# Kernel tuning notes

Hardware: AMD Instinct MI355X
Metric: run time of the kernel (lower is better)

Reference implementation:

```python
import jax, jax.numpy as jnp
import numpy as np

ALPHA = 0.01  # alpha = input_scale * weight_scale (dequant scale)
BETA = 1.0    # bias scale, fixed to 1.0 in forward


def setup_inputs() -> dict:
    key = jax.random.key(0)
    k1, k2, k3 = jax.random.split(key, 3)
    # int8 values carried in int32 containers (schema has no int8 dtype)
    x = jax.random.randint(k1, (2, 2048, 4096), -127, 128, dtype=jnp.int32)
    weight = jax.random.randint(k2, (11008, 4096), -127, 128, dtype=jnp.int32)
    bias = jax.random.normal(k3, (1, 11008), dtype=jnp.float32)
    return {"x": x, "weight": weight, "bias": bias}


def reference(x, weight, bias):
    # x: [..., K] int8 activations, weight: [N, K] int8, bias: [1, N] fp32
    x_shape = x.shape
    x2 = x.reshape(-1, x_shape[-1]).astype(jnp.int8)   # [M, K]
    w8 = weight.astype(jnp.int8)                        # [N, K]
    acc = jnp.einsum('mk,nk->mn', x2, w8, preferred_element_type=jnp.int32)
    # fused dequant scale + fp32 bias add
    y = ALPHA * acc.astype(jnp.float32) + BETA * bias   # [M, N]
    return y.reshape(*x_shape[:-1], -1)
```

## Files before the change

kernel.cpp:

```cpp
#include <hip/hip_runtime.h>


#define M_DIM 4096
#define N_DIM 11008
#define K_DIM 4096
#define BM 256
#define BN 128
#define BK 64
#define ALPHA 0.01f

typedef __attribute__((ext_vector_type(4))) int i32x4;

static __device__ __forceinline__ int pack4(int4 v) {
    return (v.x & 0xff) | ((v.y & 0xff) << 8) |
           ((v.z & 0xff) << 16) | ((unsigned)(v.w & 0xff) << 24);
}

__global__ __launch_bounds__(256) void pack_i8_kernel(
    const int4* __restrict__ x, int4* __restrict__ xout, int n16x,
    const int4* __restrict__ w, int4* __restrict__ wout, int n16_total)
{
    int i = blockIdx.x * blockDim.x + threadIdx.x;
    if (i >= n16_total) return;
    const int4* src;
    int4* dst;
    int idx;
    if (i < n16x) { src = x; dst = xout; idx = i; }
    else          { src = w; dst = wout; idx = i - n16x; }
    const int4* p = src + (size_t)4 * idx;
    int4 a = p[0], b = p[1], c = p[2], d = p[3];
    int4 r;
    r.x = pack4(a); r.y = pack4(b); r.z = pack4(c); r.w = pack4(d);
    dst[idx] = r;
}

__global__ __launch_bounds__(256, 2) void gemm_i8_kernel(
    const char* __restrict__ A,
    const char* __restrict__ B,
    const float* __restrict__ bias,
    float* __restrict__ C)
{
    __shared__ __attribute__((aligned(16))) char As[BM * BK];
    __shared__ __attribute__((aligned(16))) char Bs[BN * BK];

    const int tid  = threadIdx.x;
    const int lane = tid & 63;
    const int wave = tid >> 6;
    const int waveM = (wave >> 1) * 128;
    const int waveN = (wave & 1) * 64;
    const int bm = blockIdx.y * BM;
    const int bn = blockIdx.x * BN;

    const int lrow  = lane & 15;
    const int lquad = lane >> 4;

    const int srow = tid >> 2;
    const int scol = ((tid & 3) ^ ((tid >> 3) & 3)) * 16;
    const char* Abase = A + (size_t)(bm + srow) * K_DIM + scol;
    const char* Bbase = B + (size_t)(bn + srow) * K_DIM + scol;

    const int swq = (lquad ^ ((lrow >> 1) & 3)) * 16;

    i32x4 acc[8][4] = {};

    for (int k0 = 0; k0 < K_DIM; k0 += BK) {
#pragma unroll
        for (int c = 0; c < 4; c++)
            __builtin_amdgcn_global_load_lds(
                (const __attribute__((address_space(1))) void*)(Abase + (size_t)(64 * c) * K_DIM + k0),
                (__attribute__((address_space(3))) void*)(As + c * 4096 + tid * 16), 16, 0, 0);
#pragma unroll
        for (int c = 0; c < 2; c++)
            __builtin_amdgcn_global_load_lds(
                (const __attribute__((address_space(1))) void*)(Bbase + (size_t)(64 * c) * K_DIM + k0),
                (__attribute__((address_space(3))) void*)(Bs + c * 4096 + tid * 16), 16, 0, 0);
        __syncthreads();

        i32x4 a[8], b[4];
#pragma unroll
        for (int i = 0; i < 8; i++)
            a[i] = *(const i32x4*)(As + (waveM + i * 16 + lrow) * BK + swq);
#pragma unroll
        for (int j = 0; j < 4; j++)
            b[j] = *(const i32x4*)(Bs + (waveN + j * 16 + lrow) * BK + swq);

#pragma unroll
        for (int i = 0; i < 8; i++)
#pragma unroll
            for (int j = 0; j < 4; j++)
                acc[i][j] = __builtin_amdgcn_mfma_i32_16x16x64_i8(a[i], b[j], acc[i][j], 0, 0, 0);

        __syncthreads();
    }

#pragma unroll
    for (int i = 0; i < 8; i++) {
        const int r0 = bm + waveM + i * 16 + lquad * 4;
#pragma unroll
        for (int j = 0; j < 4; j++) {
            const int c0 = bn + waveN + j * 16 + lrow;
            const float bv = bias[c0];
#pragma unroll
            for (int r = 0; r < 4; r++) {
                C[(size_t)(r0 + r) * N_DIM + c0] = ALPHA * (float)acc[i][j][r] + bv;
            }
        }
    }
}

extern "C" void kernel_launch(void* const* d_in, const int* in_sizes, int n_in,
                              void* d_out, int out_size, void* d_ws, size_t ws_size,
                              hipStream_t stream) {
    const int*   x    = (const int*)d_in[0];
    const int*   w    = (const int*)d_in[1];
    const float* bias = (const float*)d_in[2];
    float*       out  = (float*)d_out;

    char* Ap = (char*)d_ws;
    char* Wp = (char*)d_ws + (size_t)M_DIM * K_DIM;

    const int n16x = M_DIM * K_DIM / 16;
    const int n16w = N_DIM * K_DIM / 16;
    const int n16  = n16x + n16w;
    pack_i8_kernel<<<n16 / 256, 256, 0, stream>>>(
        (const int4*)x, (int4*)Ap, n16x, (const int4*)w, (int4*)Wp, n16);

    dim3 grid(N_DIM / BN, M_DIM / BM);
    gemm_i8_kernel<<<grid, 256, 0, stream>>>(Ap, Wp, bias, out);
}
```

Measured before the change: 550.5 us.

## Double-buffer 256x256x128 int8 GEMM tiles with staged loads and XCD-aware block mapping

Grows the GEMM block tile to 256x256 with BK=128 and moves to 512 threads (8 waves). LDS becomes double-buffered, and the global-to-LDS loads for the next K tile are interleaved with four MFMA quadrant phases, using barriers, explicit vmcnt waits and s_setprio. Blocks are remapped to a 1D grid so that each XCD handles neighbouring M rows, for better L2 reuse. The aim is to hide load latency and raise arithmetic intensity, at the cost of 128KB of LDS per block and more registers, which limits occupancy.

```diff
diff --git a/kernel.cpp b/kernel.cpp
--- a/kernel.cpp
+++ b/kernel.cpp
@@ -5,8 +5,9 @@
 #define N_DIM 11008
 #define K_DIM 4096
 #define BM 256
-#define BN 128
-#define BK 64
+#define BN 256
+#define BK 128
+#define NT (K_DIM / BK)
 #define ALPHA 0.01f
 
 typedef __attribute__((ext_vector_type(4))) int i32x4;
@@ -34,63 +35,135 @@
     dst[idx] = r;
 }
 
-__global__ __launch_bounds__(256, 2) void gemm_i8_kernel(
+#define GLOAD_LDS16(g, l) __builtin_amdgcn_global_load_lds(                   \
+    (const __attribute__((address_space(1))) void*)(g),                       \
+    (__attribute__((address_space(3))) void*)(l), 16, 0, 0)
+
+#define MFMA_Q(mh, nh, aq, bq)                                                \
+    __builtin_amdgcn_s_setprio(1);                                            \
+    _Pragma("unroll")                                                         \
+    for (int i_ = 0; i_ < 4; i_++)                                            \
+        _Pragma("unroll")                                                     \
+        for (int j_ = 0; j_ < 2; j_++)                                        \
+            _Pragma("unroll")                                                 \
+            for (int k_ = 0; k_ < 2; k_++)                                    \
+                acc[(mh) * 4 + i_][(nh) * 2 + j_] =                           \
+                    __builtin_amdgcn_mfma_i32_16x16x64_i8(                    \
+                        aq[i_][k_], bq[j_][k_],                               \
+                        acc[(mh) * 4 + i_][(nh) * 2 + j_], 0, 0, 0);          \
+    __builtin_amdgcn_s_setprio(0);
+
+__global__ __launch_bounds__(512, 2) void gemm_i8_kernel(
     const char* __restrict__ A,
     const char* __restrict__ B,
     const float* __restrict__ bias,
     float* __restrict__ C)
 {
-    __shared__ __attribute__((aligned(16))) char As[BM * BK];
-    __shared__ __attribute__((aligned(16))) char Bs[BN * BK];
-
-    const int tid  = threadIdx.x;
-    const int lane = tid & 63;
-    const int wave = tid >> 6;
-    const int waveM = (wave >> 1) * 128;
-    const int waveN = (wave & 1) * 64;
-    const int bm = blockIdx.y * BM;
-    const int bn = blockIdx.x * BN;
-
+    __shared__ __attribute__((aligned(16))) char As[2][BM * BK];
+    __shared__ __attribute__((aligned(16))) char Bs[2][BN * BK];
+
+    const int tid   = threadIdx.x;
+    const int lane  = tid & 63;
+    const int wave  = tid >> 6;
+    const int waveM = (wave >> 2) * 128;
+    const int waveN = (wave & 3) * 64;
     const int lrow  = lane & 15;
     const int lquad = lane >> 4;
 
-    const int srow = tid >> 2;
-    const int scol = ((tid & 3) ^ ((tid >> 3) & 3)) * 16;
-    const char* Abase = A + (size_t)(bm + srow) * K_DIM + scol;
-    const char* Bbase = B + (size_t)(bn + srow) * K_DIM + scol;
-
-    const int swq = (lquad ^ ((lrow >> 1) & 3)) * 16;
+    const int bid = blockIdx.x;
+    const int xcd = bid & 7;
+    const int loc = bid >> 3;
+    const int bm  = (2 * xcd + (loc & 1)) * BM;
+    const int bn  = (loc >> 1) * BN;
+
+    const int srow = tid >> 3;
+    const int schk = ((tid & 7) ^ (srow & 7)) << 4;
+    const char* Asrc = A + (size_t)(bm + srow) * K_DIM + schk;
+    const char* Bsrc = B + (size_t)(bn + srow) * K_DIM + schk;
+
+    int aoff[2], boff[2];
+#pragma unroll
+    for (int ks = 0; ks < 2; ks++) {
+        const int pos = ((ks * 4 + lquad) ^ (lrow & 7)) << 4;
+        aoff[ks] = (waveM + lrow) * BK + pos;
+        boff[ks] = (waveN + lrow) * BK + pos;
+    }
 
     i32x4 acc[8][4] = {};
 
-    for (int k0 = 0; k0 < K_DIM; k0 += BK) {
-#pragma unroll
-        for (int c = 0; c < 4; c++)
-            __builtin_amdgcn_global_load_lds(
-                (const __attribute__((address_space(1))) void*)(Abase + (size_t)(64 * c) * K_DIM + k0),
-                (__attribute__((address_space(3))) void*)(As + c * 4096 + tid * 16), 16, 0, 0);
-#pragma unroll
-        for (int c = 0; c < 2; c++)
-            __builtin_amdgcn_global_load_lds(
-                (const __attribute__((address_space(1))) void*)(Bbase + (size_t)(64 * c) * K_DIM + k0),
-                (__attribute__((address_space(3))) void*)(Bs + c * 4096 + tid * 16), 16, 0, 0);
-        __syncthreads();
-
-        i32x4 a[8], b[4];
-#pragma unroll
-        for (int i = 0; i < 8; i++)
-            a[i] = *(const i32x4*)(As + (waveM + i * 16 + lrow) * BK + swq);
-#pragma unroll
-        for (int j = 0; j < 4; j++)
-            b[j] = *(const i32x4*)(Bs + (waveN + j * 16 + lrow) * BK + swq);
-
-#pragma unroll
-        for (int i = 0; i < 8; i++)
-#pragma unroll
-            for (int j = 0; j < 4; j++)
-                acc[i][j] = __builtin_amdgcn_mfma_i32_16x16x64_i8(a[i], b[j], acc[i][j], 0, 0, 0);
-
-        __syncthreads();
+    auto stage_a = [&](int buf, int t, int half) {
+        GLOAD_LDS16(Asrc + (size_t)(half * 128) * K_DIM + t * BK,
+                    &As[buf][half * 16384 + tid * 16]);
+        GLOAD_LDS16(Asrc + (size_t)(half * 128 + 64) * K_DIM + t * BK,
+                    &As[buf][half * 16384 + 8192 + tid * 16]);
+    };
+    auto stage_b = [&](int buf, int t, int half) {
+        GLOAD_LDS16(Bsrc + (size_t)(half * 128) * K_DIM + t * BK,
+                    &Bs[buf][half * 16384 + tid * 16]);
+        GLOAD_LDS16(Bsrc + (size_t)(half * 128 + 64) * K_DIM + t * BK,
+                    &Bs[buf][half * 16384 + 8192 + tid * 16]);
+    };
+
+    stage_a(0, 0, 0); stage_a(0, 0, 1);
+    stage_b(0, 0, 0); stage_b(0, 0, 1);
+    stage_a(1, 1, 0); stage_a(1, 1, 1);
+    asm volatile("s_waitcnt vmcnt(4)" ::: "memory");
+    __builtin_amdgcn_s_barrier();
+
+    for (int g = 0; g < NT; ++g) {
+        const int cur = g & 1;
+        const char* Ac = As[cur];
+        const char* Bc = Bs[cur];
+        i32x4 a0[4][2], a1[4][2], b01[2][2], b23[2][2];
+
+#pragma unroll
+        for (int i = 0; i < 4; i++)
+#pragma unroll
+            for (int ks = 0; ks < 2; ks++)
+                a0[i][ks] = *(const i32x4*)(Ac + aoff[ks] + i * 2048);
+#pragma unroll
+        for (int j = 0; j < 2; j++)
+#pragma unroll
+            for (int ks = 0; ks < 2; ks++)
+                b01[j][ks] = *(const i32x4*)(Bc + boff[ks] + j * 2048);
+        if (g + 1 < NT) { stage_b(cur ^ 1, g + 1, 0); }
+        __builtin_amdgcn_s_barrier();
+        MFMA_Q(0, 0, a0, b01);
+        __builtin_amdgcn_s_barrier();
+
+#pragma unroll
+        for (int j = 0; j < 2; j++)
+#pragma unroll
+            for (int ks = 0; ks < 2; ks++)
+                b23[j][ks] = *(const i32x4*)(Bc + boff[ks] + (j + 2) * 2048);
+        if (g + 1 < NT) { stage_b(cur ^ 1, g + 1, 1); }
+        __builtin_amdgcn_s_barrier();
+        MFMA_Q(0, 1, a0, b23);
+        __builtin_amdgcn_s_barrier();
+
+#pragma unroll
+        for (int i = 0; i < 4; i++)
+#pragma unroll
+            for (int ks = 0; ks < 2; ks++)
+                a1[i][ks] = *(const i32x4*)(Ac + aoff[ks] + (i + 4) * 2048);
+        __builtin_amdgcn_s_barrier();
+        MFMA_Q(1, 1, a1, b23);
+        __builtin_amdgcn_s_barrier();
+
+#pragma unroll
+        for (int j = 0; j < 2; j++)
+#pragma unroll
+            for (int ks = 0; ks < 2; ks++)
+                b01[j][ks] = *(const i32x4*)(Bc + boff[ks] + j * 2048);
+        if (g + 2 < NT) {
+            stage_a(cur, g + 2, 0); stage_a(cur, g + 2, 1);
+            asm volatile("s_waitcnt vmcnt(4)" ::: "memory");
+        } else {
+            asm volatile("s_waitcnt vmcnt(0)" ::: "memory");
+        }
+        __builtin_amdgcn_s_barrier();
+        MFMA_Q(1, 0, a1, b01);
+        __builtin_amdgcn_s_barrier();
     }
 
 #pragma unroll
@@ -125,6 +198,6 @@
     pack_i8_kernel<<<n16 / 256, 256, 0, stream>>>(
         (const int4*)x, (int4*)Ap, n16x, (const int4*)w, (int4*)Wp, n16);
 
-    dim3 grid(N_DIM / BN, M_DIM / BM);
-    gemm_i8_kernel<<<grid, 256, 0, stream>>>(Ap, Wp, bias, out);
-}
+    gemm_i8_kernel<<<dim3((M_DIM / BM) * (N_DIM / BN)), 512, 0, stream>>>(
+        Ap, Wp, bias, out);
+}
```

Result: no change. 548.5 us (-0.4%).

## Double-buffer LDS with 256x256x128 tiles, interleaved prefetch and XCD-aware block mapping

Applied to the files above, without the earlier changes.

The int8 GEMM is restructured around a 256x256 output tile with a K step of 128, run by 512 threads (8 waves) per block. LDS is double-buffered, and the global-to-LDS loads for the next K tile are split into four chunks. Each chunk is interleaved with MFMA groups, using explicit vmcnt waits, barriers and setprio, so memory traffic overlaps compute instead of the previous load-sync-compute loop. A 1D grid is remapped so that consecutive blocks on each XCD share A rows, and the LDS swizzle is widened to 8 chunks. The trade-off is about 128KB of LDS per block, which limits occupancy to one block per CU, plus a tightly hand-scheduled pipeline whose correctness depends on the wait counts.

```diff
diff --git a/kernel.cpp b/kernel.cpp
--- a/kernel.cpp
+++ b/kernel.cpp
@@ -5,8 +5,9 @@
 #define N_DIM 11008
 #define K_DIM 4096
 #define BM 256
-#define BN 128
-#define BK 64
+#define BN 256
+#define BK 128
+#define NT (K_DIM / BK)
 #define ALPHA 0.01f
 
 typedef __attribute__((ext_vector_type(4))) int i32x4;
@@ -34,64 +35,135 @@
     dst[idx] = r;
 }
 
-__global__ __launch_bounds__(256, 2) void gemm_i8_kernel(
+#define GA0 (s_ + 8 * (s_ >> 3))
+#define GA1 (8 + s_ + 8 * (s_ >> 3))
+#define GB0 ((s_ & 3) + 8 * (s_ >> 2))
+#define GB1 (4 + (s_ & 3) + 8 * (s_ >> 2))
+
+#define STAGE(dstArr, srcB, T, GEXPR)                                          \
+    _Pragma("unroll") for (int u_ = 0; u_ < 2; u_++) {                         \
+        const int s_ = u_ * 8 + wave;                                          \
+        const int G_ = (GEXPR);                                                \
+        __builtin_amdgcn_global_load_lds(                                      \
+            (const __attribute__((address_space(1))) void*)(                   \
+                (srcB) + (size_t)(G_ * 8 + (lane >> 3)) * K_DIM +              \
+                (size_t)(T) * BK + sch16),                                     \
+            (__attribute__((address_space(3))) void*)((dstArr) + G_ * 1024 +   \
+                                                      lane * 16),              \
+            16, 0, 0);                                                         \
+    }
+
+#define READ_A(Arr, dst, IB)                                                   \
+    _Pragma("unroll") for (int i_ = 0; i_ < 4; i_++)                           \
+        _Pragma("unroll") for (int k_ = 0; k_ < 2; k_++)                       \
+            dst[i_][k_] = *(const i32x4*)((Arr) + aoff[k_] + ((IB) + i_) * 2048);
+
+#define READ_B(Arr, dst, JB)                                                   \
+    _Pragma("unroll") for (int j_ = 0; j_ < 2; j_++)                           \
+        _Pragma("unroll") for (int k_ = 0; k_ < 2; k_++)                       \
+            dst[j_][k_] = *(const i32x4*)((Arr) + boff[k_] + ((JB) + j_) * 2048);
+
+#define MFMA_G(af, bf, IB, JB)                                                 \
+    __builtin_amdgcn_s_setprio(1);                                             \
+    _Pragma("unroll") for (int i_ = 0; i_ < 4; i_++)                           \
+        _Pragma("unroll") for (int j_ = 0; j_ < 2; j_++)                       \
+            _Pragma("unroll") for (int k_ = 0; k_ < 2; k_++)                   \
+                acc[(IB) + i_][(JB) + j_] =                                    \
+                    __builtin_amdgcn_mfma_i32_16x16x64_i8(                     \
+                        af[i_][k_], bf[j_][k_],                                \
+                        acc[(IB) + i_][(JB) + j_], 0, 0, 0);                   \
+    __builtin_amdgcn_s_setprio(0);
+
+#define VMCNT_(N) asm volatile("s_waitcnt vmcnt(" #N ")" ::: "memory")
+#define VMCNT(N) VMCNT_(N)
+
+#define TILE(CA, CB, NA, NB, T, B01C, B01N, STG, NRD, V1, V2, V3, V4)          \
+    {                                                                          \
+                            \
+        if (STG) { STAGE(NA, Abase, (T) + 1, GA0); }                           \
+        VMCNT(V1);                                                             \
+        __builtin_amdgcn_s_barrier();                                          \
+        READ_B(CB, rb23, 2);                                                   \
+        MFMA_G(ra0, B01C, 0, 0);                                               \
+        __builtin_amdgcn_s_barrier();                                          \
+                             \
+        if (STG) { STAGE(NB, Bbase, (T) + 1, GB0); }                           \
+        VMCNT(V2);                                                             \
+        __builtin_amdgcn_s_barrier();                                          \
+        READ_A(CA, ra1, 4);                                                    \
+        MFMA_G(ra0, rb23, 0, 2);                                               \
+        __builtin_amdgcn_s_barrier();                                          \
+                                         \
+        if (STG) { STAGE(NB, Bbase, (T) + 1, GB1); }                           \
+        VMCNT(V3);                                                             \
+        __builtin_amdgcn_s_barrier();                                          \
+        MFMA_G(ra1, rb23, 4, 2);                                               \
+        __builtin_amdgcn_s_barrier();                                          \
+          \
+        if (STG) { STAGE(NA, Abase, (T) + 1, GA1); }                           \
+        VMCNT(V4);                                                             \
+        __builtin_amdgcn_s_barrier();                                          \
+        if (NRD) { READ_A(NA, ra0, 0); READ_B(NB, B01N, 0); }                  \
+        MFMA_G(ra1, B01C, 4, 0);                                               \
+        __builtin_amdgcn_s_barrier();                                          \
+    }
+
+__global__ __launch_bounds__(512, 2) void gemm_i8_kernel(
     const char* __restrict__ A,
     const char* __restrict__ B,
     const float* __restrict__ bias,
     float* __restrict__ C)
 {
-    __shared__ __attribute__((aligned(16))) char As[BM * BK];
-    __shared__ __attribute__((aligned(16))) char Bs[BN * BK];
-
-    const int tid  = threadIdx.x;
-    const int lane = tid & 63;
-    const int wave = tid >> 6;
-    const int waveM = (wave >> 1) * 128;
-    const int waveN = (wave & 1) * 64;
-    const int bm = blockIdx.y * BM;
-    const int bn = blockIdx.x * BN;
-
+    __shared__ __attribute__((aligned(16))) char As0[BM * BK];
+    __shared__ __attribute__((aligned(16))) char Bs0[BN * BK];
+    __shared__ __attribute__((aligned(16))) char As1[BM * BK];
+    __shared__ __attribute__((aligned(16))) char Bs1[BN * BK];
+
+    const int tid   = threadIdx.x;
+    const int lane  = tid & 63;
+    const int wave  = tid >> 6;
+    const int waveM = (wave >> 2) * 128;
+    const int waveN = (wave & 3) * 64;
     const int lrow  = lane & 15;
     const int lquad = lane >> 4;
 
-    const int srow = tid >> 2;
-    const int scol = ((tid & 3) ^ ((tid >> 3) & 3)) * 16;
-    const char* Abase = A + (size_t)(bm + srow) * K_DIM + scol;
-    const char* Bbase = B + (size_t)(bn + srow) * K_DIM + scol;
-
-    const int swq = (lquad ^ ((lrow >> 1) & 3)) * 16;
+    const int bid = blockIdx.x;
+    const int xcd = bid & 7;
+    const int loc = bid >> 3;
+    const int bm  = (2 * xcd + (loc & 1)) * BM;
+    const int bn  = (loc >> 1) * BN;
+
+    const int sch16 = ((lane & 7) ^ ((lane >> 3) & 7)) << 4;
+    const char* Abase = A + (size_t)bm * K_DIM;
+    const char* Bbase = B + (size_t)bn * K_DIM;
+
+    int aoff[2], boff[2];
+#pragma unroll
+    for (int ks = 0; ks < 2; ks++) {
+        const int pos = ((ks * 4 + lquad) ^ (lrow & 7)) << 4;
+        aoff[ks] = (waveM + lrow) * BK + pos;
+        boff[ks] = (waveN + lrow) * BK + pos;
+    }
 
     i32x4 acc[8][4] = {};
-
-    for (int k0 = 0; k0 < K_DIM; k0 += BK) {
-#pragma unroll
-        for (int c = 0; c < 4; c++)
-            __builtin_amdgcn_global_load_lds(
-                (const __attribute__((address_space(1))) void*)(Abase + (size_t)(64 * c) * K_DIM + k0),
-                (__attribute__((address_space(3))) void*)(As + c * 4096 + tid * 16), 16, 0, 0);
-#pragma unroll
-        for (int c = 0; c < 2; c++)
-            __builtin_amdgcn_global_load_lds(
-                (const __attribute__((address_space(1))) void*)(Bbase + (size_t)(64 * c) * K_DIM + k0),
-                (__attribute__((address_space(3))) void*)(Bs + c * 4096 + tid * 16), 16, 0, 0);
-        __syncthreads();
-
-        i32x4 a[8], b[4];
-#pragma unroll
-        for (int i = 0; i < 8; i++)
-            a[i] = *(const i32x4*)(As + (waveM + i * 16 + lrow) * BK + swq);
-#pragma unroll
-        for (int j = 0; j < 4; j++)
-            b[j] = *(const i32x4*)(Bs + (waveN + j * 16 + lrow) * BK + swq);
-
-#pragma unroll
-        for (int i = 0; i < 8; i++)
-#pragma unroll
-            for (int j = 0; j < 4; j++)
-                acc[i][j] = __builtin_amdgcn_mfma_i32_16x16x64_i8(a[i], b[j], acc[i][j], 0, 0, 0);
-
-        __syncthreads();
-    }
+    i32x4 ra0[4][2], ra1[4][2], rb01A[2][2], rb01B[2][2], rb23[2][2];
+
+    STAGE(As0, Abase, 0, GA0);
+    STAGE(Bs0, Bbase, 0, GB0);
+    STAGE(Bs0, Bbase, 0, GB1);
+    STAGE(As0, Abase, 0, GA1);
+    VMCNT(0);
+    __builtin_amdgcn_s_barrier();
+    READ_A(As0, ra0, 0);
+    READ_B(Bs0, rb01A, 0);
+
+#pragma unroll 1
+    for (int t = 0; t < NT - 2; t += 2) {
+        TILE(As0, Bs0, As1, Bs1, t,     rb01A, rb01B, 1, 1, 4, 4, 4, 4);
+        TILE(As1, Bs1, As0, Bs0, t + 1, rb01B, rb01A, 1, 1, 4, 4, 4, 4);
+    }
+    TILE(As0, Bs0, As1, Bs1, NT - 2, rb01A, rb01B, 1, 1, 4, 4, 4, 4);
+    TILE(As1, Bs1, As0, Bs0, NT - 1, rb01B, rb01A, 0, 0, 2, 0, 0, 0);
 
 #pragma unroll
     for (int i = 0; i < 8; i++) {
@@ -125,6 +197,6 @@
     pack_i8_kernel<<<n16 / 256, 256, 0, stream>>>(
         (const int4*)x, (int4*)Ap, n16x, (const int4*)w, (int4*)Wp, n16);
 
-    dim3 grid(N_DIM / BN, M_DIM / BM);
-    gemm_i8_kernel<<<grid, 256, 0, stream>>>(Ap, Wp, bias, out);
-}
+    gemm_i8_kernel<<<dim3((M_DIM / BM) * (N_DIM / BN)), 512, 0, stream>>>(
+        Ap, Wp, bias, out);
+}
```

Result: slower. 739.9 us (+34.4%).
